# Kernel optimization log

Hardware: AMD Instinct MI355X
Metric: run time of the kernel (lower is better)

Reference implementation:

```python
import jax, jax.numpy as jnp
import numpy as np

B, C, R = 100000, 64, 128

def setup_inputs() -> dict:
    key = jax.random.key(0)
    k1, k2, k3 = jax.random.split(key, 3)
    return {
        "compressed_vectors": jax.random.normal(k1, (B, C, 3), dtype=jnp.float32),
        "W1": jax.random.normal(k2, (C, 32), dtype=jnp.float32) * (1.0 / np.sqrt(C)),
        "b1": jnp.zeros((32,), dtype=jnp.float32),
        "W2": jax.random.normal(k3, (32, R * C), dtype=jnp.float32) * (1.0 / np.sqrt(32)),
        "b2": jnp.zeros((R * C,), dtype=jnp.float32),
    }

def reference(compressed_vectors, W1, b1, W2, b2):
    # scalar invariants: L2 norm over Cartesian axis -> [B, C]
    scalar_invariants = jnp.linalg.norm(compressed_vectors, axis=-1)
    # tiny MLP: C -> 32 -> R*C
    h = jax.nn.relu(scalar_invariants @ W1 + b1)
    scalar_weights = (h @ W2 + b2).reshape(-1, R, C)  # [B, R, C]
    # outer product of vectors: [B, C, 3, 3]
    rank2_tensors = jnp.einsum('bci,bcj->bcij', compressed_vectors, compressed_vectors)
    # weighted bilinear contraction over channels: [B, R, 3, 3]
    reconstructed_tensors = jnp.einsum('brc,bcij->brij', scalar_weights, rank2_tensors)
    return reconstructed_tensors
```

## Files before the change

### kernel.cpp

```cpp
#include <hip/hip_runtime.h>
#include <hip/hip_bf16.h>


#define NB 16
#define RT 16

typedef float f32x4 __attribute__((ext_vector_type(4)));
typedef __bf16 bf16x8 __attribute__((ext_vector_type(8)));

static __device__ __forceinline__ unsigned short bf_bits(float f) {
  __hip_bfloat16 h = __float2bfloat16(f);
  return *reinterpret_cast<const unsigned short*>(&h);
}
static __device__ __forceinline__ unsigned int pack_bf2(float a, float b) {
  return (unsigned int)bf_bits(a) | ((unsigned int)bf_bits(b) << 16);
}

__global__ void prep_w2t(const float* __restrict__ W2, unsigned short* __restrict__ w2t) {
  int rc = blockIdx.x * 256 + threadIdx.x;
  unsigned int u[16];
#pragma unroll
  for (int kp = 0; kp < 16; ++kp) {
    float a = W2[(size_t)(2 * kp) * 8192 + rc];
    float b = W2[(size_t)(2 * kp + 1) * 8192 + rc];
    u[kp] = pack_bf2(a, b);
  }
  unsigned int* dst = reinterpret_cast<unsigned int*>(w2t + (size_t)rc * 32);
#pragma unroll
  for (int j = 0; j < 16; ++j) dst[j] = u[j];
}

__global__ __launch_bounds__(256, 4)
void erl_main(const float* __restrict__ v, const float* __restrict__ W1,
              const float* __restrict__ b1, const float* __restrict__ b2,
              const unsigned short* __restrict__ w2t, float* __restrict__ out) {
  __shared__ __align__(16) char smem[37376];
  unsigned short* W_lds = reinterpret_cast<unsigned short*>(smem);
  float* W1_lds = reinterpret_cast<float*>(smem);
  float* s_lds = reinterpret_cast<float*>(smem + 8192);
  unsigned short* h_lds = reinterpret_cast<unsigned short*>(smem + 12544);

  const int t = threadIdx.x;
  const int b0 = blockIdx.x * NB;
  const int lane = t & 63;
  const int wid = t >> 6;
  const int x = lane >> 4;
  const int col = lane & 15;

  {
    const f32x4* w1v = reinterpret_cast<const f32x4*>(W1);
    f32x4* w1d = reinterpret_cast<f32x4*>(W1_lds);
    w1d[t] = w1v[t];
    w1d[t + 256] = w1v[t + 256];
  }
#pragma unroll
  for (int j = 0; j < 4; ++j) {
    int p = t + j * 256;
    int b = p >> 6, c = p & 63;
    const float* vp = v + ((size_t)(b0 + b) * 64 + c) * 3;
    float vx = vp[0], vy = vp[1], vz = vp[2];
    s_lds[b * 68 + c] = sqrtf(vx * vx + vy * vy + vz * vz);
  }

  const int seff = (col < 9) ? col : 8;
  const int ei = seff / 3;
  const int ej = seff - ei * 3;
  bf16x8 mfr[4][2];
#pragma unroll
  for (int i = 0; i < 4; ++i) {
    int b = wid * 4 + i;
#pragma unroll
    for (int ch = 0; ch < 2; ++ch) {
      const float* vb = v + ((size_t)(b0 + b) * 64 + ch * 32 + x * 8) * 3;
      union { f32x4 q[6]; float f[24]; } u;
#pragma unroll
      for (int l = 0; l < 6; ++l) u.q[l] = reinterpret_cast<const f32x4*>(vb)[l];
      bf16x8 fr;
#pragma unroll
      for (int e = 0; e < 8; ++e) {
        float vx = u.f[e * 3 + 0], vy = u.f[e * 3 + 1], vz = u.f[e * 3 + 2];
        float pa = (ei == 0) ? vx : ((ei == 1) ? vy : vz);
        float pb = (ej == 0) ? vx : ((ej == 1) ? vy : vz);
        fr[e] = (__bf16)(pa * pb);
      }
      mfr[i][ch] = fr;
    }
  }
  __syncthreads();

  {
    int b = t >> 4, kk = t & 15;
    float a0 = b1[kk], a1 = b1[kk + 16];
    const f32x4* srow = reinterpret_cast<const f32x4*>(s_lds + b * 68);
#pragma unroll
    for (int c4 = 0; c4 < 16; ++c4) {
      f32x4 sv = srow[c4];
#pragma unroll
      for (int uu = 0; uu < 4; ++uu) {
        int c = c4 * 4 + uu;
        a0 = fmaf(sv[uu], W1_lds[c * 32 + kk], a0);
        a1 = fmaf(sv[uu], W1_lds[c * 32 + kk + 16], a1);
      }
    }
    h_lds[b * 32 + kk] = bf_bits(fmaxf(a0, 0.f));
    h_lds[b * 32 + kk + 16] = bf_bits(fmaxf(a1, 0.f));
  }
  __syncthreads();

  bf16x8 hfrag = *reinterpret_cast<const bf16x8*>(&h_lds[col * 32 + x * 8]);
  __syncthreads();

  const unsigned short* ap = w2t + (size_t)wid * 8192 + col * 32 + x * 8;
  const float* b2p = b2 + wid * 256 + x * 4;
  const int w_widx = col * 1168 + wid * 288 + x * 4;
  const int w_ridx = wid * 4672 + col * 72 + x * 8;
  float* op[4];
#pragma unroll
  for (int i = 0; i < 4; ++i)
    op[i] = out + (size_t)(b0 + wid * 4 + i) * 1152 + x * 36 + col;
  const bool do_store = (col < 9);

  bf16x8 afA[4], afB[4];
  f32x4 bsA[4];
#pragma unroll
  for (int jj = 0; jj < 4; ++jj) {
    afA[jj] = *reinterpret_cast<const bf16x8*>(ap + jj * 512);
    bsA[jj] = *reinterpret_cast<const f32x4*>(b2p + jj * 16);
  }

  for (int rt = 0; rt < 8; ++rt) {
#pragma unroll
    for (int ck = 0; ck < 4; ++ck) {
      if (ck < 3) {
#pragma unroll
        for (int jj = 0; jj < 4; ++jj) {
          int tt = (ck + 1) * 4 + jj;
          afB[jj] = *reinterpret_cast<const bf16x8*>(ap + tt * 512);
        }
      }
#pragma unroll
      for (int jj = 0; jj < 4; ++jj) {
        f32x4 acc = (ck == 0) ? bsA[jj]
                  : *reinterpret_cast<const f32x4*>(b2p + (ck * 4 + jj) * 16);
        acc = __builtin_amdgcn_mfma_f32_16x16x32_bf16(afA[jj], hfrag, acc, 0, 0, 0);
        unsigned int* wp = reinterpret_cast<unsigned int*>(&W_lds[w_widx + ck * 72 + jj * 16]);
        wp[0] = pack_bf2(acc[0], acc[1]);
        wp[1] = pack_bf2(acc[2], acc[3]);
      }
      if (ck < 3) {
#pragma unroll
        for (int jj = 0; jj < 4; ++jj) afA[jj] = afB[jj];
      }
    }
    ap += 32768; b2p += 1024;
    __syncthreads();

    if (rt < 7) {
#pragma unroll
      for (int jj = 0; jj < 4; ++jj) {
        afA[jj] = *reinterpret_cast<const bf16x8*>(ap + jj * 512);
        bsA[jj] = *reinterpret_cast<const f32x4*>(b2p + jj * 16);
      }
    }

#pragma unroll
    for (int i = 0; i < 4; ++i) {
      bf16x8 a20 = *reinterpret_cast<const bf16x8*>(&W_lds[w_ridx + i * 1168]);
      bf16x8 a21 = *reinterpret_cast<const bf16x8*>(&W_lds[w_ridx + i * 1168 + 32]);
      f32x4 acc2 = {0.f, 0.f, 0.f, 0.f};
      acc2 = __builtin_amdgcn_mfma_f32_16x16x32_bf16(a20, mfr[i][0], acc2, 0, 0, 0);
      acc2 = __builtin_amdgcn_mfma_f32_16x16x32_bf16(a21, mfr[i][1], acc2, 0, 0, 0);
      if (do_store) {
        float* p = op[i];
        p[0] = acc2[0]; p[9] = acc2[1]; p[18] = acc2[2]; p[27] = acc2[3];
      }
      op[i] += 144;
    }
    __syncthreads();
  }
}

extern "C" void kernel_launch(void* const* d_in, const int* in_sizes, int n_in,
                              void* d_out, int out_size, void* d_ws, size_t ws_size,
                              hipStream_t stream) {
  const float* v  = (const float*)d_in[0];
  const float* W1 = (const float*)d_in[1];
  const float* b1 = (const float*)d_in[2];
  const float* W2 = (const float*)d_in[3];
  const float* b2 = (const float*)d_in[4];
  float* out = (float*)d_out;

  unsigned short* w2t = (unsigned short*)d_ws;

  prep_w2t<<<32, 256, 0, stream>>>(W2, w2t);
  erl_main<<<100000 / NB, 256, 0, stream>>>(v, W1, b1, b2, w2t, out);
}
```

Before: 401.5 us.

## Split hidden-layer MLP into separate kernel and spread R tiles across blocks

Adds a prep_h kernel that computes the norms and the first MLP layer once per batch element, writing bf16 hidden activations to workspace. The main kernel now gives each block a single R tile (8x more blocks) instead of looping over all 8 tiles, which removes the in-loop barriers and the per-block MLP prologue. The cost is that the vector data and outer-product fragments are loaded and built 8 times per batch group instead of once, plus an extra kernel launch and a workspace round trip for h.

```diff
diff --git a/kernel.cpp b/kernel.cpp
--- a/kernel.cpp
+++ b/kernel.cpp
@@ -2,11 +2,9 @@
 #include <hip/hip_bf16.h>
 
 
-#define NB 16
-#define RT 16
-
 typedef float f32x4 __attribute__((ext_vector_type(4)));
 typedef __bf16 bf16x8 __attribute__((ext_vector_type(8)));
+typedef unsigned int u32x4 __attribute__((ext_vector_type(4)));
 
 static __device__ __forceinline__ unsigned short bf_bits(float f) {
   __hip_bfloat16 h = __float2bfloat16(f);
@@ -30,38 +28,79 @@
   for (int j = 0; j < 16; ++j) dst[j] = u[j];
 }
 
+__global__ void prep_h(const float* __restrict__ v, const float* __restrict__ W1,
+                       const float* __restrict__ b1, unsigned short* __restrict__ hws) {
+  __shared__ float v_lds[64 * 192];
+  __shared__ float s_lds[64 * 68];
+  __shared__ float W1T[32 * 68];
+  const int t = threadIdx.x;
+  const int b0 = blockIdx.x * 64;
+  const int rem = (100000 - b0 < 64) ? (100000 - b0) : 64;
+
+#pragma unroll
+  for (int j = 0; j < 8; ++j) {
+    int p = t + j * 256;
+    W1T[(p & 31) * 68 + (p >> 5)] = W1[p];
+  }
+  {
+    const f32x4* src = reinterpret_cast<const f32x4*>(v + (size_t)b0 * 192);
+    f32x4* dst = reinterpret_cast<f32x4*>(v_lds);
+    const int nq = rem * 48;
+#pragma unroll
+    for (int j = 0; j < 12; ++j) {
+      int p = t + j * 256;
+      if (p < nq) dst[p] = src[p];
+    }
+  }
+  __syncthreads();
+
+  const int b = t >> 2, kq = t & 3;
+#pragma unroll
+  for (int cc = 0; cc < 16; ++cc) {
+    int c = kq * 16 + cc;
+    float vx = v_lds[b * 192 + c * 3];
+    float vy = v_lds[b * 192 + c * 3 + 1];
+    float vz = v_lds[b * 192 + c * 3 + 2];
+    s_lds[b * 68 + c] = sqrtf(vx * vx + vy * vy + vz * vz);
+  }
+  __syncthreads();
+
+  if (b < rem) {
+    float acc[8];
+#pragma unroll
+    for (int e = 0; e < 8; ++e) acc[e] = b1[kq * 8 + e];
+#pragma unroll
+    for (int c4 = 0; c4 < 16; ++c4) {
+      f32x4 sv = *reinterpret_cast<const f32x4*>(&s_lds[b * 68 + c4 * 4]);
+#pragma unroll
+      for (int e = 0; e < 8; ++e) {
+        f32x4 wr = *reinterpret_cast<const f32x4*>(&W1T[(kq * 8 + e) * 68 + c4 * 4]);
+#pragma unroll
+        for (int u = 0; u < 4; ++u) acc[e] = fmaf(sv[u], wr[u], acc[e]);
+      }
+    }
+    u32x4 pk;
+#pragma unroll
+    for (int p2 = 0; p2 < 4; ++p2)
+      pk[p2] = pack_bf2(fmaxf(acc[2 * p2], 0.f), fmaxf(acc[2 * p2 + 1], 0.f));
+    *reinterpret_cast<u32x4*>(hws + (size_t)(b0 + b) * 32 + kq * 8) = pk;
+  }
+}
+
 __global__ __launch_bounds__(256, 4)
-void erl_main(const float* __restrict__ v, const float* __restrict__ W1,
-              const float* __restrict__ b1, const float* __restrict__ b2,
-              const unsigned short* __restrict__ w2t, float* __restrict__ out) {
-  __shared__ __align__(16) char smem[37376];
-  unsigned short* W_lds = reinterpret_cast<unsigned short*>(smem);
-  float* W1_lds = reinterpret_cast<float*>(smem);
-  float* s_lds = reinterpret_cast<float*>(smem + 8192);
-  unsigned short* h_lds = reinterpret_cast<unsigned short*>(smem + 12544);
+void erl_main(const float* __restrict__ v, const float* __restrict__ b2,
+              const unsigned short* __restrict__ w2t,
+              const unsigned short* __restrict__ hws, float* __restrict__ out) {
+  __shared__ __align__(16) unsigned short W_lds[16 * 1168];
 
   const int t = threadIdx.x;
-  const int b0 = blockIdx.x * NB;
-  const int lane = t & 63;
-  const int wid = t >> 6;
-  const int x = lane >> 4;
-  const int col = lane & 15;
+  const int wid = t >> 6, lane = t & 63;
+  const int x = lane >> 4, col = lane & 15;
+  const int bid = blockIdx.x;
+  const int rt = bid & 7;
+  const int b0 = (bid >> 3) * 16;
 
-  {
-    const f32x4* w1v = reinterpret_cast<const f32x4*>(W1);
-    f32x4* w1d = reinterpret_cast<f32x4*>(W1_lds);
-    w1d[t] = w1v[t];
-    w1d[t + 256] = w1v[t + 256];
-  }
-#pragma unroll
-  for (int j = 0; j < 4; ++j) {
-    int p = t + j * 256;
-    int b = p >> 6, c = p & 63;
-    const float* vp = v + ((size_t)(b0 + b) * 64 + c) * 3;
-    float vx = vp[0], vy = vp[1], vz = vp[2];
-    s_lds[b * 68 + c] = sqrtf(vx * vx + vy * vy + vz * vz);
-  }
-
+  bf16x8 hfrag = *reinterpret_cast<const bf16x8*>(&hws[(size_t)(b0 + col) * 32 + x * 8]);
   const int seff = (col < 9) ? col : 8;
   const int ei = seff / 3;
   const int ej = seff - ei * 3;
@@ -86,97 +125,49 @@
       mfr[i][ch] = fr;
     }
   }
-  __syncthreads();
 
-  {
-    int b = t >> 4, kk = t & 15;
-    float a0 = b1[kk], a1 = b1[kk + 16];
-    const f32x4* srow = reinterpret_cast<const f32x4*>(s_lds + b * 68);
+  const unsigned short* ap = w2t + ((size_t)(rt * 1024 + wid * 256 + col)) * 32 + x * 8;
+  const float* b2p = b2 + rt * 1024 + wid * 256 + x * 4;
+  const int w_widx = col * 1168 + wid * 288 + x * 4;
+
+  bf16x8 afA[4], afB[4];
 #pragma unroll
-    for (int c4 = 0; c4 < 16; ++c4) {
-      f32x4 sv = srow[c4];
+  for (int j = 0; j < 4; ++j) afA[j] = *reinterpret_cast<const bf16x8*>(ap + j * 512);
 #pragma unroll
-      for (int uu = 0; uu < 4; ++uu) {
-        int c = c4 * 4 + uu;
-        a0 = fmaf(sv[uu], W1_lds[c * 32 + kk], a0);
-        a1 = fmaf(sv[uu], W1_lds[c * 32 + kk + 16], a1);
-      }
+  for (int g = 0; g < 4; ++g) {
+    if (g < 3) {
+#pragma unroll
+      for (int j = 0; j < 4; ++j)
+        afB[j] = *reinterpret_cast<const bf16x8*>(ap + ((g + 1) * 4 + j) * 512);
     }
-    h_lds[b * 32 + kk] = bf_bits(fmaxf(a0, 0.f));
-    h_lds[b * 32 + kk + 16] = bf_bits(fmaxf(a1, 0.f));
+#pragma unroll
+    for (int j = 0; j < 4; ++j) {
+      int tt = g * 4 + j;
+      f32x4 acc = *reinterpret_cast<const f32x4*>(b2p + tt * 16);
+      acc = __builtin_amdgcn_mfma_f32_16x16x32_bf16(afA[j], hfrag, acc, 0, 0, 0);
+      unsigned int* wp = reinterpret_cast<unsigned int*>(&W_lds[w_widx + (tt >> 2) * 72 + (tt & 3) * 16]);
+      wp[0] = pack_bf2(acc[0], acc[1]);
+      wp[1] = pack_bf2(acc[2], acc[3]);
+    }
+    if (g < 3) {
+      afA[0] = afB[0]; afA[1] = afB[1]; afA[2] = afB[2]; afA[3] = afB[3];
+    }
   }
   __syncthreads();
 
-  bf16x8 hfrag = *reinterpret_cast<const bf16x8*>(&h_lds[col * 32 + x * 8]);
-  __syncthreads();
-
-  const unsigned short* ap = w2t + (size_t)wid * 8192 + col * 32 + x * 8;
-  const float* b2p = b2 + wid * 256 + x * 4;
-  const int w_widx = col * 1168 + wid * 288 + x * 4;
   const int w_ridx = wid * 4672 + col * 72 + x * 8;
-  float* op[4];
+  const bool do_store = (col < 9);
 #pragma unroll
-  for (int i = 0; i < 4; ++i)
-    op[i] = out + (size_t)(b0 + wid * 4 + i) * 1152 + x * 36 + col;
-  const bool do_store = (col < 9);
-
-  bf16x8 afA[4], afB[4];
-  f32x4 bsA[4];
-#pragma unroll
-  for (int jj = 0; jj < 4; ++jj) {
-    afA[jj] = *reinterpret_cast<const bf16x8*>(ap + jj * 512);
-    bsA[jj] = *reinterpret_cast<const f32x4*>(b2p + jj * 16);
-  }
-
-  for (int rt = 0; rt < 8; ++rt) {
-#pragma unroll
-    for (int ck = 0; ck < 4; ++ck) {
-      if (ck < 3) {
-#pragma unroll
-        for (int jj = 0; jj < 4; ++jj) {
-          int tt = (ck + 1) * 4 + jj;
-          afB[jj] = *reinterpret_cast<const bf16x8*>(ap + tt * 512);
-        }
-      }
-#pragma unroll
-      for (int jj = 0; jj < 4; ++jj) {
-        f32x4 acc = (ck == 0) ? bsA[jj]
-                  : *reinterpret_cast<const f32x4*>(b2p + (ck * 4 + jj) * 16);
-        acc = __builtin_amdgcn_mfma_f32_16x16x32_bf16(afA[jj], hfrag, acc, 0, 0, 0);
-        unsigned int* wp = reinterpret_cast<unsigned int*>(&W_lds[w_widx + ck * 72 + jj * 16]);
-        wp[0] = pack_bf2(acc[0], acc[1]);
-        wp[1] = pack_bf2(acc[2], acc[3]);
-      }
-      if (ck < 3) {
-#pragma unroll
-        for (int jj = 0; jj < 4; ++jj) afA[jj] = afB[jj];
-      }
+  for (int i = 0; i < 4; ++i) {
+    bf16x8 a0 = *reinterpret_cast<const bf16x8*>(&W_lds[w_ridx + i * 1168]);
+    bf16x8 a1 = *reinterpret_cast<const bf16x8*>(&W_lds[w_ridx + i * 1168 + 32]);
+    f32x4 o = {0.f, 0.f, 0.f, 0.f};
+    o = __builtin_amdgcn_mfma_f32_16x16x32_bf16(a0, mfr[i][0], o, 0, 0, 0);
+    o = __builtin_amdgcn_mfma_f32_16x16x32_bf16(a1, mfr[i][1], o, 0, 0, 0);
+    if (do_store) {
+      float* p = out + (size_t)(b0 + wid * 4 + i) * 1152 + rt * 144 + x * 36 + col;
+      p[0] = o[0]; p[9] = o[1]; p[18] = o[2]; p[27] = o[3];
     }
-    ap += 32768; b2p += 1024;
-    __syncthreads();
-
-    if (rt < 7) {
-#pragma unroll
-      for (int jj = 0; jj < 4; ++jj) {
-        afA[jj] = *reinterpret_cast<const bf16x8*>(ap + jj * 512);
-        bsA[jj] = *reinterpret_cast<const f32x4*>(b2p + jj * 16);
-      }
-    }
-
-#pragma unroll
-    for (int i = 0; i < 4; ++i) {
-      bf16x8 a20 = *reinterpret_cast<const bf16x8*>(&W_lds[w_ridx + i * 1168]);
-      bf16x8 a21 = *reinterpret_cast<const bf16x8*>(&W_lds[w_ridx + i * 1168 + 32]);
-      f32x4 acc2 = {0.f, 0.f, 0.f, 0.f};
-      acc2 = __builtin_amdgcn_mfma_f32_16x16x32_bf16(a20, mfr[i][0], acc2, 0, 0, 0);
-      acc2 = __builtin_amdgcn_mfma_f32_16x16x32_bf16(a21, mfr[i][1], acc2, 0, 0, 0);
-      if (do_store) {
-        float* p = op[i];
-        p[0] = acc2[0]; p[9] = acc2[1]; p[18] = acc2[2]; p[27] = acc2[3];
-      }
-      op[i] += 144;
-    }
-    __syncthreads();
   }
 }
 
@@ -191,7 +182,9 @@
   float* out = (float*)d_out;
 
   unsigned short* w2t = (unsigned short*)d_ws;
+  unsigned short* hws = (unsigned short*)d_ws + 8192 * 32;
 
   prep_w2t<<<32, 256, 0, stream>>>(W2, w2t);
-  erl_main<<<100000 / NB, 256, 0, stream>>>(v, W1, b1, b2, w2t, out);
+  prep_h<<<1563, 256, 0, stream>>>(v, W1, b1, hws);
+  erl_main<<<50000, 256, 0, stream>>>(v, b2, w2t, hws, out);
 }
```

Measured after the change: 1.410 ms. 3.51x slower.
